# Kernel tuning notes

Hardware: AMD Instinct MI355X
Metric: run time of the kernel (lower is better)

## Reference

```python
import jax, jax.numpy as jnp
import numpy as np
import math

N_HEADS = 16
DIM = 1024
HEAD_DIM = DIM // N_HEADS
BS, QLEN = 4, 2048


def setup_inputs() -> dict:
    key = jax.random.key(0)
    ks = jax.random.split(key, 10)
    s = 0.02
    return {
        "input": jax.random.normal(ks[0], (BS, QLEN, DIM), dtype=jnp.float32),
        "mask": jnp.ones((BS, QLEN), dtype=jnp.int32),
        "wq": jax.random.normal(ks[1], (DIM, DIM), dtype=jnp.float32) * s,
        "bq": jax.random.normal(ks[2], (DIM,), dtype=jnp.float32) * s,
        "wk": jax.random.normal(ks[3], (DIM, DIM), dtype=jnp.float32) * s,
        "bk": jax.random.normal(ks[4], (DIM,), dtype=jnp.float32) * s,
        "wv": jax.random.normal(ks[5], (DIM, DIM), dtype=jnp.float32) * s,
        "bv": jax.random.normal(ks[6], (DIM,), dtype=jnp.float32) * s,
        "wo": jax.random.normal(ks[7], (DIM, DIM), dtype=jnp.float32) * s,
        "bo": jax.random.normal(ks[8], (DIM,), dtype=jnp.float32) * s,
    }


def reference(input, mask, wq, bq, wk, bk, wv, bv, wo, bo):
    bs, qlen, dim = input.shape
    # torch Linear: y = x @ W.T + b
    def proj(x, w, b):
        y = jnp.einsum("bsd,ed->bse", x, w) + b
        # [bs, seq, n_heads, head_dim] -> [bs, n_heads, seq, head_dim]
        return y.reshape(bs, qlen, N_HEADS, HEAD_DIM).transpose(0, 2, 1, 3)

    q = proj(input, wq, bq) / math.sqrt(HEAD_DIM)
    k = proj(input, wk, bk)
    v = proj(input, wv, bv)

    # scores: [bs, n_heads, qlen, klen]
    scores = jnp.einsum("bhqd,bhkd->bhqk", q, k)
    pad = (mask == 0)[:, None, None, :]  # (bs,1,1,klen)
    scores = jnp.where(pad, -jnp.inf, scores)
    weights = jax.nn.softmax(scores.astype(jnp.float32), axis=-1).astype(scores.dtype)
    # dropout p=0 (eval mode) -> identity
    context = jnp.einsum("bhqk,bhkd->bhqd", weights, v)
    context = context.transpose(0, 2, 1, 3).reshape(bs, qlen, dim)
    out = jnp.einsum("bsd,ed->bse", context, wo) + bo
    return out
```

## Files before the change

### kernel.cpp

```cpp
#include <hip/hip_runtime.h>
#include <cstdint>

typedef unsigned int u32;
typedef unsigned short u16;
typedef __attribute__((ext_vector_type(8))) short bf16x8;
typedef __attribute__((ext_vector_type(4))) float f32x4;

#define QSCALE 0.1803368801111204f

typedef const void __attribute__((address_space(1)))* gas1p;
typedef void __attribute__((address_space(3)))* las3p;

__device__ __forceinline__ void gload_lds16(const void* g, void* l) {
  __builtin_amdgcn_global_load_lds((gas1p)g, (las3p)l, 16, 0, 0);
}

#if __has_builtin(__builtin_amdgcn_exp2f)
#define EXP2F(x) __builtin_amdgcn_exp2f(x)
#else
#define EXP2F(x) exp2f(x)
#endif

__device__ __forceinline__ u16 f2bf(float f) {
  __bf16 h = (__bf16)f;
  return __builtin_bit_cast(u16, h);
}

__global__ void cvt_kernel(const float* __restrict__ src, u16* __restrict__ dst, int n4) {
  int i = blockIdx.x * blockDim.x + threadIdx.x;
  int stride = gridDim.x * blockDim.x;
  for (; i < n4; i += stride) {
    float4 f = ((const float4*)src)[i];
    ushort4 o;
    o.x = f2bf(f.x); o.y = f2bf(f.y); o.z = f2bf(f.z); o.w = f2bf(f.w);
    ((ushort4*)dst)[i] = o;
  }
}

__global__ void cvt4_kernel(const float* __restrict__ s0, const float* __restrict__ s1,
                            const float* __restrict__ s2, const float* __restrict__ s3,
                            u16* __restrict__ d0, u16* __restrict__ d1,
                            u16* __restrict__ d2, u16* __restrict__ d3, int n4) {
  const float* s; u16* d;
  switch (blockIdx.y) {
    case 0: s = s0; d = d0; break;
    case 1: s = s1; d = d1; break;
    case 2: s = s2; d = d2; break;
    default: s = s3; d = d3; break;
  }
  int i = blockIdx.x * blockDim.x + threadIdx.x;
  int stride = gridDim.x * blockDim.x;
  for (; i < n4; i += stride) {
    float4 f = ((const float4*)s)[i];
    ushort4 o;
    o.x = f2bf(f.x); o.y = f2bf(f.y); o.z = f2bf(f.z); o.w = f2bf(f.w);
    ((ushort4*)d)[i] = o;
  }
}

__global__ void maskflag_kernel(const int* __restrict__ mask, int* __restrict__ flags) {
  int id = blockIdx.x * blockDim.x + threadIdx.x;
  if (id < 128) {
    int b = id >> 5, ch = id & 31;
    const int4* p = (const int4*)(mask + b * 2048 + ch * 64);
    int ok = 1;
#pragma unroll
    for (int j = 0; j < 16; j++) {
      int4 v = p[j];
      ok &= (v.x != 0) & (v.y != 0) & (v.z != 0) & (v.w != 0);
    }
    flags[id] = ok;
  }
}

__global__ __launch_bounds__(256, 2)
void gemm_qkv(const u16* __restrict__ X,
              const u16* __restrict__ Wq, const u16* __restrict__ Wk, const u16* __restrict__ Wv,
              const float* __restrict__ bq, const float* __restrict__ bk, const float* __restrict__ bv,
              u16* __restrict__ Qh, u16* __restrict__ Kh, u16* __restrict__ Vp) {
  __shared__ u16 smem[16384];
  const int t = threadIdx.x;
  const int lane = t & 63;
  const int wid = t >> 6;
  const int g = lane >> 4, q16 = lane & 15;
  const int wr = wid >> 1, wc = wid & 1;
  const int n0 = blockIdx.x * 128;
  const int m0 = blockIdx.y * 128;
  const int z = blockIdx.z;
  const u16* B = (z == 0) ? Wq : (z == 1) ? Wk : Wv;
  const float* bias = (z == 0) ? bq : (z == 1) ? bk : bv;

  auto stage = [&](int buf, int k0) {
#pragma unroll
    for (int i = 0; i < 2; i++) {
      int idx = i * 256 + t;
      int row = idx >> 2, sl = idx & 3;
      int ss = sl ^ ((row >> 1) & 3);
      gload_lds16(X + (size_t)(m0 + row) * 1024 + k0 + ss * 8, (char*)(smem + buf * 4096) + idx * 16);
      gload_lds16(B + (size_t)(n0 + row) * 1024 + k0 + ss * 8, (char*)(smem + 8192 + buf * 4096) + idx * 16);
    }
  };

  f32x4 acc[4][4] = {};
  stage(0, 0);
  __syncthreads();
  for (int kt = 0; kt < 32; kt++) {
    if (kt < 31) stage((kt + 1) & 1, (kt + 1) * 32);
    const u16* Ab = smem + (kt & 1) * 4096;
    const u16* Bb = smem + 8192 + (kt & 1) * 4096;
    bf16x8 af[4], bfr[4];
#pragma unroll
    for (int mi = 0; mi < 4; mi++) {
      int row = wr * 64 + mi * 16 + q16;
      int ps = g ^ ((row >> 1) & 3);
      af[mi] = *(const bf16x8*)((const char*)Ab + row * 64 + ps * 16);
      int rowb = wc * 64 + mi * 16 + q16;
      int psb = g ^ ((rowb >> 1) & 3);
      bfr[mi] = *(const bf16x8*)((const char*)Bb + rowb * 64 + psb * 16);
    }
#pragma unroll
    for (int mi = 0; mi < 4; mi++)
#pragma unroll
      for (int ni = 0; ni < 4; ni++)
        acc[mi][ni] = __builtin_amdgcn_mfma_f32_16x16x32_bf16(af[mi], bfr[ni], acc[mi][ni], 0, 0, 0);
    __syncthreads();
  }

  if (z == 2) {
    u16* T = smem;
    const int TP = 132;
#pragma unroll 1
    for (int half = 0; half < 2; half++) {
      __syncthreads();
      if (wc == half) {
#pragma unroll
        for (int ni = 0; ni < 4; ni++) {
          int dloc = ni * 16 + q16;
          float bv_ = bias[n0 + half * 64 + dloc];
#pragma unroll
          for (int mi = 0; mi < 4; mi++) {
            ushort4 o;
            o.x = f2bf(acc[mi][ni][0] + bv_);
            o.y = f2bf(acc[mi][ni][1] + bv_);
            o.z = f2bf(acc[mi][ni][2] + bv_);
            o.w = f2bf(acc[mi][ni][3] + bv_);
            *(ushort4*)&T[dloc * TP + wr * 64 + mi * 16 + g * 4] = o;
          }
        }
      }
      __syncthreads();
      {
        int dloc = t >> 2, c = t & 3;
        int h = (n0 >> 6) + half;
        int b = m0 >> 11;
        size_t gbase = ((size_t)(b * 16 + h) * 64 + dloc) * 2048 + (m0 & 2047)
                     + (c >> 1) * 64 + (c & 1) * 32;
#pragma unroll
        for (int j = 0; j < 8; j++) {
          ushort4 v = *(const ushort4*)&T[dloc * TP + c * 32 + j * 4];
          *(ushort4*)&Vp[gbase + (j & 3) * 8 + (j >> 2) * 4] = v;
        }
      }
    }
    return;
  }

#pragma unroll
  for (int ni = 0; ni < 4; ni++) {
    int col = n0 + wc * 64 + ni * 16 + q16;
    float bv_ = bias[col];
    int h = col >> 6, d = col & 63;
#pragma unroll
    for (int mi = 0; mi < 4; mi++) {
#pragma unroll
      for (int r = 0; r < 4; r++) {
        int row = m0 + wr * 64 + mi * 16 + g * 4 + r;
        int b = row >> 11, sq = row & 2047;
        float v = acc[mi][ni][r] + bv_;
        if (z == 0) {
          Qh[(((size_t)(b * 16 + h)) * 2048 + sq) * 64 + d] = f2bf(v * QSCALE);
        } else {
          Kh[(((size_t)(b * 16 + h)) * 2048 + sq) * 64 + d] = f2bf(v);
        }
      }
    }
  }
}

__global__ __launch_bounds__(256, 2)
void gemm_out(const u16* __restrict__ X, const u16* __restrict__ W,
              const float* __restrict__ bias, float* __restrict__ Out) {
  __shared__ u16 As[2][128 * 32];
  __shared__ u16 Bs[2][128 * 32];
  const int t = threadIdx.x;
  const int lane = t & 63;
  const int wid = t >> 6;
  const int g = lane >> 4, q16 = lane & 15;
  const int wr = wid >> 1, wc = wid & 1;
  const int n0 = blockIdx.x * 128;
  const int m0 = blockIdx.y * 128;

  auto stage = [&](int buf, int k0) {
#pragma unroll
    for (int i = 0; i < 2; i++) {
      int idx = i * 256 + t;
      int row = idx >> 2, sl = idx & 3;
      int ss = sl ^ ((row >> 1) & 3);
      gload_lds16(X + (size_t)(m0 + row) * 1024 + k0 + ss * 8, (char*)&As[buf][0] + idx * 16);
      gload_lds16(W + (size_t)(n0 + row) * 1024 + k0 + ss * 8, (char*)&Bs[buf][0] + idx * 16);
    }
  };

  f32x4 acc[4][4] = {};
  stage(0, 0);
  __syncthreads();
  for (int kt = 0; kt < 32; kt++) {
    if (kt < 31) stage((kt + 1) & 1, (kt + 1) * 32);
    const u16* Ab = &As[kt & 1][0];
    const u16* Bb = &Bs[kt & 1][0];
    bf16x8 af[4], bfr[4];
#pragma unroll
    for (int mi = 0; mi < 4; mi++) {
      int row = wr * 64 + mi * 16 + q16;
      int ps = g ^ ((row >> 1) & 3);
      af[mi] = *(const bf16x8*)((const char*)Ab + row * 64 + ps * 16);
      int rowb = wc * 64 + mi * 16 + q16;
      int psb = g ^ ((rowb >> 1) & 3);
      bfr[mi] = *(const bf16x8*)((const char*)Bb + rowb * 64 + psb * 16);
    }
#pragma unroll
    for (int mi = 0; mi < 4; mi++)
#pragma unroll
      for (int ni = 0; ni < 4; ni++)
        acc[mi][ni] = __builtin_amdgcn_mfma_f32_16x16x32_bf16(af[mi], bfr[ni], acc[mi][ni], 0, 0, 0);
    __syncthreads();
  }

#pragma unroll
  for (int ni = 0; ni < 4; ni++) {
    int col = n0 + wc * 64 + ni * 16 + q16;
    float bv_ = bias[col];
#pragma unroll
    for (int mi = 0; mi < 4; mi++) {
#pragma unroll
      for (int r = 0; r < 4; r++) {
        int row = m0 + wr * 64 + mi * 16 + g * 4 + r;
        Out[(size_t)row * 1024 + col] = acc[mi][ni][r] + bv_;
      }
    }
  }
}

__global__ __launch_bounds__(256, 4)
void attn_kernel(const u16* __restrict__ Qh, const u16* __restrict__ Kh,
                 const u16* __restrict__ Vp, const int* __restrict__ mask,
                 const int* __restrict__ mflags, u16* __restrict__ ctx) {
  __shared__ u16 Ks[2][64 * 64];
  __shared__ u16 Vs[2][64 * 64];
  const int t = threadIdx.x;
  const int lane = t & 63;
  const int w = t >> 6;
  const int g = lane >> 4, q16 = lane & 15;
  const int flat = blockIdx.y * 16 + blockIdx.x;
  const int xcd = flat & 7, slot = flat >> 3;
  const int bh = xcd + 8 * (slot >> 4);
  const int qb = slot & 15;
  const int b = bh >> 4, h = bh & 15;

  bf16x8 qf[2][2];
#pragma unroll
  for (int qg = 0; qg < 2; qg++) {
    const u16* qp = Qh + ((size_t)bh * 2048 + qb * 128 + w * 32 + qg * 16 + q16) * 64;
    qf[qg][0] = *(const bf16x8*)(qp + g * 8);
    qf[qg][1] = *(const bf16x8*)(qp + 32 + g * 8);
  }

  auto stage = [&](int buf, int kv0) {
#pragma unroll
    for (int i = 0; i < 2; i++) {
      int idx = i * 256 + t;
      int row = idx >> 3, sl = idx & 7;
      int ss = sl ^ (row & 7);
      gload_lds16(Kh + ((size_t)bh * 2048 + kv0 + row) * 64 + ss * 8, (char*)&Ks[buf][0] + idx * 16);
      gload_lds16(Vp + ((size_t)bh * 64 + row) * 2048 + kv0 + ss * 8, (char*)&Vs[buf][0] + idx * 16);
    }
  };

  f32x4 oacc[2][4] = {};
  float lsum[2] = {0.f, 0.f};
  const int4* mrow = (const int4*)(mask + b * 2048);
  const int* mf = mflags + b * 32;

  stage(0, 0);
  __syncthreads();

  for (int it = 0; it < 32; it++) {
    const int kv0 = it * 64;
    if (it < 31) stage((it + 1) & 1, kv0 + 64);
    const u16* Kb = &Ks[it & 1][0];
    const u16* Vb = &Vs[it & 1][0];

    f32x4 sac[2][4] = {};
#pragma unroll
    for (int ks = 0; ks < 2; ks++) {
#pragma unroll
      for (int mb = 0; mb < 4; mb++) {
        int row = mb * 16 + q16;
        int ps = (ks * 4 + g) ^ (row & 7);
        bf16x8 kf = *(const bf16x8*)((const char*)Kb + row * 128 + ps * 16);
        sac[0][mb] = __builtin_amdgcn_mfma_f32_16x16x32_bf16(kf, qf[0][ks], sac[0][mb], 0, 0, 0);
        sac[1][mb] = __builtin_amdgcn_mfma_f32_16x16x32_bf16(kf, qf[1][ks], sac[1][mb], 0, 0, 0);
      }
    }

    const int mfit = mf[it];
    bf16x8 pf[2][2];
#pragma unroll
    for (int qg = 0; qg < 2; qg++) {
      float p[16];
      if (mfit) {
#pragma unroll
        for (int mb = 0; mb < 4; mb++) {
          p[mb * 4 + 0] = EXP2F(sac[qg][mb][0]);
          p[mb * 4 + 1] = EXP2F(sac[qg][mb][1]);
          p[mb * 4 + 2] = EXP2F(sac[qg][mb][2]);
          p[mb * 4 + 3] = EXP2F(sac[qg][mb][3]);
        }
      } else {
#pragma unroll
        for (int mb = 0; mb < 4; mb++) {
          int4 mv = mrow[(kv0 + mb * 16 + g * 4) >> 2];
          p[mb * 4 + 0] = mv.x ? EXP2F(sac[qg][mb][0]) : 0.f;
          p[mb * 4 + 1] = mv.y ? EXP2F(sac[qg][mb][1]) : 0.f;
          p[mb * 4 + 2] = mv.z ? EXP2F(sac[qg][mb][2]) : 0.f;
          p[mb * 4 + 3] = mv.w ? EXP2F(sac[qg][mb][3]) : 0.f;
        }
      }
      float ps_ = 0.f;
#pragma unroll
      for (int j = 0; j < 16; j++) ps_ += p[j];
      lsum[qg] += ps_;
#pragma unroll
      for (int ks = 0; ks < 2; ks++)
#pragma unroll
        for (int j = 0; j < 8; j++) pf[qg][ks][j] = (short)f2bf(p[8 * ks + j]);
    }

#pragma unroll
    for (int ks = 0; ks < 2; ks++) {
#pragma unroll
      for (int nb = 0; nb < 4; nb++) {
        int row = nb * 16 + q16;
        int ps = (ks * 4 + g) ^ (row & 7);
        bf16x8 vf = *(const bf16x8*)((const char*)Vb + row * 128 + ps * 16);
        oacc[0][nb] = __builtin_amdgcn_mfma_f32_16x16x32_bf16(pf[0][ks], vf, oacc[0][nb], 0, 0, 0);
        oacc[1][nb] = __builtin_amdgcn_mfma_f32_16x16x32_bf16(pf[1][ks], vf, oacc[1][nb], 0, 0, 0);
      }
    }
    __syncthreads();
  }

#pragma unroll
  for (int qg = 0; qg < 2; qg++) {
    float ls = lsum[qg];
    ls += __shfl_xor(ls, 16);
    ls += __shfl_xor(ls, 32);
    float rinv = (ls > 0.f) ? 1.f / ls : 0.f;
    float r0 = __shfl(rinv, (g << 4) + g * 4 + 0);
    float r1 = __shfl(rinv, (g << 4) + g * 4 + 1);
    float r2 = __shfl(rinv, (g << 4) + g * 4 + 2);
    float r3 = __shfl(rinv, (g << 4) + g * 4 + 3);
#pragma unroll
    for (int nb = 0; nb < 4; nb++) {
      int col = h * 64 + nb * 16 + q16;
      size_t base = ((size_t)b * 2048 + qb * 128 + w * 32 + qg * 16 + g * 4) * 1024 + col;
      ctx[base + (size_t)0 * 1024] = f2bf(oacc[qg][nb][0] * r0);
      ctx[base + (size_t)1 * 1024] = f2bf(oacc[qg][nb][1] * r1);
      ctx[base + (size_t)2 * 1024] = f2bf(oacc[qg][nb][2] * r2);
      ctx[base + (size_t)3 * 1024] = f2bf(oacc[qg][nb][3] * r3);
    }
  }
}

extern "C" void kernel_launch(void* const* d_in, const int* in_sizes, int n_in,
                              void* d_out, int out_size, void* d_ws, size_t ws_size,
                              hipStream_t stream) {
  (void)in_sizes; (void)n_in; (void)out_size; (void)ws_size;
  const float* input = (const float*)d_in[0];
  const int* mask = (const int*)d_in[1];
  const float* wq = (const float*)d_in[2];
  const float* bq = (const float*)d_in[3];
  const float* wk = (const float*)d_in[4];
  const float* bk = (const float*)d_in[5];
  const float* wv = (const float*)d_in[6];
  const float* bv = (const float*)d_in[7];
  const float* wo = (const float*)d_in[8];
  const float* bo = (const float*)d_in[9];
  float* out = (float*)d_out;

  u16* xb = (u16*)d_ws;
  u16* wqb = xb + (size_t)8192 * 1024;
  u16* wkb = wqb + (size_t)1024 * 1024;
  u16* wvb = wkb + (size_t)1024 * 1024;
  u16* wob = wvb + (size_t)1024 * 1024;
  u16* Qh = wob + (size_t)1024 * 1024;
  u16* Kh = Qh + (size_t)64 * 2048 * 64;
  u16* Vp = Kh + (size_t)64 * 2048 * 64;
  int* mflags = (int*)(Vp + (size_t)64 * 64 * 2048);
  u16* ctx = xb;

  cvt_kernel<<<2048, 256, 0, stream>>>(input, xb, 8192 * 1024 / 4);
  cvt4_kernel<<<dim3(256, 4), 256, 0, stream>>>(wq, wk, wv, wo, wqb, wkb, wvb, wob,
                                                1024 * 1024 / 4);
  maskflag_kernel<<<1, 128, 0, stream>>>(mask, mflags);

  gemm_qkv<<<dim3(8, 64, 3), 256, 0, stream>>>(xb, wqb, wkb, wvb, bq, bk, bv, Qh, Kh, Vp);
  attn_kernel<<<dim3(16, 64), 256, 0, stream>>>(Qh, Kh, Vp, mask, mflags, ctx);
  gemm_out<<<dim3(8, 64), 256, 0, stream>>>(ctx, wob, bo, out);
}
```

Baseline: 284.4 us.

## Fuse Q and K projections per block, remap blocks per XCD, prioritize attention MFMA

The QKV GEMM now computes Q and K together in one block, so each staged X tile is reused for two weight tiles. V is handled by a separate set of blocks, which shrinks the grid from 3 to 2 z-slices but leaves the Q/K blocks with twice the accumulators and more LDS. Block indices in both GEMMs are remapped so that blocks sharing rows of X land on the same XCD, aiming for better L2 reuse. The attention kernel wraps its MFMA sections in s_setprio to favour matrix issue across waves. The main risk is that higher register and LDS use lowers occupancy and that Q/K and V blocks become unbalanced.

```diff
diff --git a/kernel.cpp b/kernel.cpp
--- a/kernel.cpp
+++ b/kernel.cpp
@@ -78,34 +78,98 @@
               const u16* __restrict__ Wq, const u16* __restrict__ Wk, const u16* __restrict__ Wv,
               const float* __restrict__ bq, const float* __restrict__ bk, const float* __restrict__ bv,
               u16* __restrict__ Qh, u16* __restrict__ Kh, u16* __restrict__ Vp) {
-  __shared__ u16 smem[16384];
+  __shared__ u16 smem[24576];
   const int t = threadIdx.x;
   const int lane = t & 63;
   const int wid = t >> 6;
   const int g = lane >> 4, q16 = lane & 15;
   const int wr = wid >> 1, wc = wid & 1;
-  const int n0 = blockIdx.x * 128;
-  const int m0 = blockIdx.y * 128;
-  const int z = blockIdx.z;
-  const u16* B = (z == 0) ? Wq : (z == 1) ? Wk : Wv;
-  const float* bias = (z == 0) ? bq : (z == 1) ? bk : bv;
-
-  auto stage = [&](int buf, int k0) {
-#pragma unroll
-    for (int i = 0; i < 2; i++) {
-      int idx = i * 256 + t;
+  const int i = blockIdx.x + (blockIdx.y << 3) + (blockIdx.z << 9);
+  const int xcd = i & 7, j = i >> 3;
+  const int wy = (xcd << 3) + (j & 7);
+  const int wx = (j >> 3) & 7;
+  const int z = j >> 6;
+  const int n0 = wx * 128;
+  const int m0 = wy * 128;
+
+  if (z == 0) {
+    auto stage = [&](int buf, int k0) {
+#pragma unroll
+      for (int i2 = 0; i2 < 2; i2++) {
+        int idx = i2 * 256 + t;
+        int row = idx >> 2, sl = idx & 3;
+        int ss = sl ^ ((row >> 1) & 3);
+        gload_lds16(X + (size_t)(m0 + row) * 1024 + k0 + ss * 8, (char*)(smem + buf * 4096) + idx * 16);
+        gload_lds16(Wq + (size_t)(n0 + row) * 1024 + k0 + ss * 8, (char*)(smem + 8192 + buf * 4096) + idx * 16);
+        gload_lds16(Wk + (size_t)(n0 + row) * 1024 + k0 + ss * 8, (char*)(smem + 16384 + buf * 4096) + idx * 16);
+      }
+    };
+
+    f32x4 accq[4][4] = {}, acck[4][4] = {};
+    stage(0, 0);
+    __syncthreads();
+    for (int kt = 0; kt < 32; kt++) {
+      if (kt < 31) stage((kt + 1) & 1, (kt + 1) * 32);
+      const u16* Ab = smem + (kt & 1) * 4096;
+      const u16* Bqb = smem + 8192 + (kt & 1) * 4096;
+      const u16* Bkb = smem + 16384 + (kt & 1) * 4096;
+      bf16x8 af[4], bqf[4], bkf[4];
+#pragma unroll
+      for (int mi = 0; mi < 4; mi++) {
+        int row = wr * 64 + mi * 16 + q16;
+        int ps = g ^ ((row >> 1) & 3);
+        af[mi] = *(const bf16x8*)((const char*)Ab + row * 64 + ps * 16);
+        int rowb = wc * 64 + mi * 16 + q16;
+        int psb = g ^ ((rowb >> 1) & 3);
+        bqf[mi] = *(const bf16x8*)((const char*)Bqb + rowb * 64 + psb * 16);
+        bkf[mi] = *(const bf16x8*)((const char*)Bkb + rowb * 64 + psb * 16);
+      }
+#pragma unroll
+      for (int mi = 0; mi < 4; mi++)
+#pragma unroll
+        for (int ni = 0; ni < 4; ni++) {
+          accq[mi][ni] = __builtin_amdgcn_mfma_f32_16x16x32_bf16(af[mi], bqf[ni], accq[mi][ni], 0, 0, 0);
+          acck[mi][ni] = __builtin_amdgcn_mfma_f32_16x16x32_bf16(af[mi], bkf[ni], acck[mi][ni], 0, 0, 0);
+        }
+      __syncthreads();
+    }
+
+#pragma unroll
+    for (int ni = 0; ni < 4; ni++) {
+      int col = n0 + wc * 64 + ni * 16 + q16;
+      float bqv = bq[col], bkv = bk[col];
+      int h = col >> 6, d = col & 63;
+#pragma unroll
+      for (int mi = 0; mi < 4; mi++) {
+#pragma unroll
+        for (int r = 0; r < 4; r++) {
+          int row = m0 + wr * 64 + mi * 16 + g * 4 + r;
+          int b = row >> 11, sq = row & 2047;
+          size_t base = (((size_t)(b * 16 + h)) * 2048 + sq) * 64 + d;
+          Qh[base] = f2bf((accq[mi][ni][r] + bqv) * QSCALE);
+          Kh[base] = f2bf(acck[mi][ni][r] + bkv);
+        }
+      }
+    }
+    return;
+  }
+
+  auto stagev = [&](int buf, int k0) {
+#pragma unroll
+    for (int i2 = 0; i2 < 2; i2++) {
+      int idx = i2 * 256 + t;
       int row = idx >> 2, sl = idx & 3;
       int ss = sl ^ ((row >> 1) & 3);
       gload_lds16(X + (size_t)(m0 + row) * 1024 + k0 + ss * 8, (char*)(smem + buf * 4096) + idx * 16);
-      gload_lds16(B + (size_t)(n0 + row) * 1024 + k0 + ss * 8, (char*)(smem + 8192 + buf * 4096) + idx * 16);
+      gload_lds16(Wv + (size_t)(n0 + row) * 1024 + k0 + ss * 8, (char*)(smem + 8192 + buf * 4096) + idx * 16);
     }
   };
 
   f32x4 acc[4][4] = {};
-  stage(0, 0);
+  stagev(0, 0);
   __syncthreads();
   for (int kt = 0; kt < 32; kt++) {
-    if (kt < 31) stage((kt + 1) & 1, (kt + 1) * 32);
+    if (kt < 31) stagev((kt + 1) & 1, (kt + 1) * 32);
     const u16* Ab = smem + (kt & 1) * 4096;
     const u16* Bb = smem + 8192 + (kt & 1) * 4096;
     bf16x8 af[4], bfr[4];
@@ -126,7 +190,7 @@
     __syncthreads();
   }
 
-  if (z == 2) {
+  {
     u16* T = smem;
     const int TP = 132;
 #pragma unroll 1
@@ -136,7 +200,7 @@
 #pragma unroll
         for (int ni = 0; ni < 4; ni++) {
           int dloc = ni * 16 + q16;
-          float bv_ = bias[n0 + half * 64 + dloc];
+          float bv_ = bv[n0 + half * 64 + dloc];
 #pragma unroll
           for (int mi = 0; mi < 4; mi++) {
             ushort4 o;
@@ -156,31 +220,9 @@
         size_t gbase = ((size_t)(b * 16 + h) * 64 + dloc) * 2048 + (m0 & 2047)
                      + (c >> 1) * 64 + (c & 1) * 32;
 #pragma unroll
-        for (int j = 0; j < 8; j++) {
-          ushort4 v = *(const ushort4*)&T[dloc * TP + c * 32 + j * 4];
-          *(ushort4*)&Vp[gbase + (j & 3) * 8 + (j >> 2) * 4] = v;
-        }
-      }
-    }
-    return;
-  }
-
-#pragma unroll
-  for (int ni = 0; ni < 4; ni++) {
-    int col = n0 + wc * 64 + ni * 16 + q16;
-    float bv_ = bias[col];
-    int h = col >> 6, d = col & 63;
-#pragma unroll
-    for (int mi = 0; mi < 4; mi++) {
-#pragma unroll
-      for (int r = 0; r < 4; r++) {
-        int row = m0 + wr * 64 + mi * 16 + g * 4 + r;
-        int b = row >> 11, sq = row & 2047;
-        float v = acc[mi][ni][r] + bv_;
-        if (z == 0) {
-          Qh[(((size_t)(b * 16 + h)) * 2048 + sq) * 64 + d] = f2bf(v * QSCALE);
-        } else {
-          Kh[(((size_t)(b * 16 + h)) * 2048 + sq) * 64 + d] = f2bf(v);
+        for (int jj = 0; jj < 8; jj++) {
+          ushort4 v = *(const ushort4*)&T[dloc * TP + c * 32 + jj * 4];
+          *(ushort4*)&Vp[gbase + (jj & 3) * 8 + (jj >> 2) * 4] = v;
         }
       }
     }
@@ -197,13 +239,17 @@
   const int wid = t >> 6;
   const int g = lane >> 4, q16 = lane & 15;
   const int wr = wid >> 1, wc = wid & 1;
-  const int n0 = blockIdx.x * 128;
-  const int m0 = blockIdx.y * 128;
+  const int i = blockIdx.x + (blockIdx.y << 3);
+  const int xcd = i & 7, j = i >> 3;
+  const int wy = (xcd << 3) + (j & 7);
+  const int wx = j >> 3;
+  const int n0 = wx * 128;
+  const int m0 = wy * 128;
 
   auto stage = [&](int buf, int k0) {
 #pragma unroll
-    for (int i = 0; i < 2; i++) {
-      int idx = i * 256 + t;
+    for (int i2 = 0; i2 < 2; i2++) {
+      int idx = i2 * 256 + t;
       int row = idx >> 2, sl = idx & 3;
       int ss = sl ^ ((row >> 1) & 3);
       gload_lds16(X + (size_t)(m0 + row) * 1024 + k0 + ss * 8, (char*)&As[buf][0] + idx * 16);
@@ -301,6 +347,7 @@
     const u16* Vb = &Vs[it & 1][0];
 
     f32x4 sac[2][4] = {};
+    __builtin_amdgcn_s_setprio(1);
 #pragma unroll
     for (int ks = 0; ks < 2; ks++) {
 #pragma unroll
@@ -312,6 +359,7 @@
         sac[1][mb] = __builtin_amdgcn_mfma_f32_16x16x32_bf16(kf, qf[1][ks], sac[1][mb], 0, 0, 0);
       }
     }
+    __builtin_amdgcn_s_setprio(0);
 
     const int mfit = mf[it];
     bf16x8 pf[2][2];
@@ -338,14 +386,15 @@
       }
       float ps_ = 0.f;
 #pragma unroll
-      for (int j = 0; j < 16; j++) ps_ += p[j];
+      for (int jj = 0; jj < 16; jj++) ps_ += p[jj];
       lsum[qg] += ps_;
 #pragma unroll
       for (int ks = 0; ks < 2; ks++)
 #pragma unroll
-        for (int j = 0; j < 8; j++) pf[qg][ks][j] = (short)f2bf(p[8 * ks + j]);
-    }
-
+        for (int jj = 0; jj < 8; jj++) pf[qg][ks][jj] = (short)f2bf(p[8 * ks + jj]);
+    }
+
+    __builtin_amdgcn_s_setprio(1);
 #pragma unroll
     for (int ks = 0; ks < 2; ks++) {
 #pragma unroll
@@ -357,6 +406,7 @@
         oacc[1][nb] = __builtin_amdgcn_mfma_f32_16x16x32_bf16(pf[1][ks], vf, oacc[1][nb], 0, 0, 0);
       }
     }
+    __builtin_amdgcn_s_setprio(0);
     __syncthreads();
   }
 
@@ -414,7 +464,7 @@
                                                 1024 * 1024 / 4);
   maskflag_kernel<<<1, 128, 0, stream>>>(mask, mflags);
 
-  gemm_qkv<<<dim3(8, 64, 3), 256, 0, stream>>>(xb, wqb, wkb, wvb, bq, bk, bv, Qh, Kh, Vp);
+  gemm_qkv<<<dim3(8, 64, 2), 256, 0, stream>>>(xb, wqb, wkb, wvb, bq, bk, bv, Qh, Kh, Vp);
   attn_kernel<<<dim3(16, 64), 256, 0, stream>>>(Qh, Kh, Vp, mask, mflags, ctx);
   gemm_out<<<dim3(8, 64), 256, 0, stream>>>(ctx, wob, bo, out);
 }
```

After: 283.4 us. Within noise of the previous version (-0.4%).
